# Kernel tuning notes

Hardware: AMD Instinct MI355X
Metric: run time of the kernel (lower is better)

The kernel has to match this reference:

```python
import jax, jax.numpy as jnp
import numpy as np

N, IN_F, OUT_F = 4096, 4096, 4096
THRESH = 0.05


def setup_inputs() -> dict:
    key = jax.random.key(0)
    k_x, k_w = jax.random.split(key)
    last_out = jax.random.normal(k_x, (N, IN_F), dtype=jnp.float32)
    # learned weight buffer, [out_features, in_features] like torch Linear
    weight = jax.random.normal(k_w, (OUT_F, IN_F), dtype=jnp.float32) * (1.0 / np.sqrt(IN_F))
    threshold = jnp.float32(THRESH)
    return {"last_out": last_out, "weight": weight, "threshold": threshold}


def reference(last_out, weight, threshold):
    # rtp_linear: runtime threshold pruning — activations with |x| <= threshold
    # are skipped (treated as zero) in the matmul. Bias buffer is unused
    # (dead code in the original forward).
    x = jnp.where(jnp.abs(last_out) > threshold, last_out, 0.0)
    # y[n, o] = sum_i x[n, i] * W[o, i]
    return jnp.einsum("ni,oi->no", x, weight)
```

## Files before the change

### kernel.cpp

```cpp
#include <hip/hip_runtime.h>
#include <hip/hip_bf16.h>

#define M_DIM 4096
#define N_DIM 4096
#define K_DIM 4096

typedef __attribute__((ext_vector_type(8))) __bf16 bf16x8;
typedef __attribute__((ext_vector_type(8))) short short8;
typedef __attribute__((ext_vector_type(8))) unsigned short ushort8;
typedef __attribute__((ext_vector_type(4))) float f32x4;

__device__ __forceinline__ void gload_lds16(const void* g, void* l) {
    __builtin_amdgcn_global_load_lds(
        (const __attribute__((address_space(1))) void*)g,
        (__attribute__((address_space(3))) void*)l,
        16, 0, 0);
}

__device__ __forceinline__ bf16x8 ld8(const unsigned short* p) {
    short8 r = *reinterpret_cast<const short8*>(p);
    return __builtin_bit_cast(bf16x8, r);
}

__global__ void prune_cvt2(const float* __restrict__ x,
                           const float* __restrict__ w,
                           unsigned short* __restrict__ xb,
                           unsigned short* __restrict__ wb,
                           const float* __restrict__ thrp, int n8) {
    const float thr = thrp[0];
    const int stride = gridDim.x * blockDim.x;
    const int total = 2 * n8;
    for (int idx = blockIdx.x * blockDim.x + threadIdx.x; idx < total; idx += stride) {
        const bool isx = idx < n8;
        const int j = isx ? idx : idx - n8;
        const float* src = isx ? x : w;
        unsigned short* dst = isx ? xb : wb;
        const float te = isx ? thr : -1.0f;
        const float4* p = reinterpret_cast<const float4*>(src) + 2 * (size_t)j;
        float4 v0 = p[0];
        float4 v1 = p[1];
        float v[8] = {v0.x, v0.y, v0.z, v0.w, v1.x, v1.y, v1.z, v1.w};
        ushort8 o;
#pragma unroll
        for (int e = 0; e < 8; ++e) {
            float f = v[e];
            f = (fabsf(f) > te) ? f : 0.0f;
            __hip_bfloat16 hh = __float2bfloat16(f);
            o[e] = *reinterpret_cast<unsigned short*>(&hh);
        }
        *reinterpret_cast<ushort8*>(dst + 8 * (size_t)j) = o;
    }
}

__global__ __launch_bounds__(512, 2) void gemm_8phase(
        const unsigned short* __restrict__ A,
        const unsigned short* __restrict__ B,
        float* __restrict__ C) {
    __shared__ __align__(16) unsigned short lds[65536];

    const int tid  = threadIdx.x;
    const int lane = tid & 63;
    const int wid  = tid >> 6;
    const int wr   = wid >> 2;
    const int wc   = wid & 3;

    const int bid = blockIdx.x;
    const int swz = (bid & 7) * 32 + (bid >> 3);
    const int bm = (swz >> 4) * 256;
    const int bn = (swz & 15) * 256;

    const int g  = tid & 255;
    const int ah = tid >> 8;
    const int arow = bm + ah * 128 + (g >> 3);
    const int acol = 8 * ((g & 7) ^ ((g >> 3) & 7));
    const unsigned short* Asrc = A + (size_t)arow * K_DIM + acol;
    const int AdstE = ah * 8192 + g * 8;

    const int h = lane + 64 * wr;
    const int brow = bn + wc * 64 + (h >> 3);
    const int bcol = 8 * ((h & 7) ^ ((h >> 3) & 7));
    const unsigned short* Bsrc = B + (size_t)brow * K_DIM + bcol;
    const int BdstE = wc * 4096 + h * 8;

#define SA(dstb, j, kg) gload_lds16(Asrc + (size_t)(32*(j))*K_DIM + (kg), (dstb) + AdstE + 2048*(j))
#define SB(dstb, j, kg) gload_lds16(Bsrc + (size_t)(16*(j))*K_DIM + (kg), (dstb) + BdstE + 1024*(j))

    const int fr  = lane & 15;
    const int kq4 = lane >> 4;
    const int rowOffA = (wr * 128 + fr) * 64;
    const int rowOffB = (wc * 64 + fr) * 64;
    const int sk0 = 8 * ((kq4    ) ^ (fr & 7));
    const int sk1 = 8 * ((kq4 + 4) ^ (fr & 7));

    f32x4 acc[8][4] = {};

    bf16x8 bfE[4][2], bfO[4][2];

#define MFMA16(q, BF, A00, A10, A01, A11)                                                          \
    __builtin_amdgcn_s_setprio(1);                                                                 \
    _Pragma("unroll")                                                                              \
    for (int n = 0; n < 4; ++n) {                                                                  \
        acc[2*(q)][n]   = __builtin_amdgcn_mfma_f32_16x16x32_bf16(A00, BF[n][0], acc[2*(q)][n], 0, 0, 0);   \
        acc[2*(q)+1][n] = __builtin_amdgcn_mfma_f32_16x16x32_bf16(A10, BF[n][0], acc[2*(q)+1][n], 0, 0, 0); \
    }                                                                                              \
    _Pragma("unroll")                                                                              \
    for (int n = 0; n < 4; ++n) {                                                                  \
        acc[2*(q)][n]   = __builtin_amdgcn_mfma_f32_16x16x32_bf16(A01, BF[n][1], acc[2*(q)][n], 0, 0, 0);   \
        acc[2*(q)+1][n] = __builtin_amdgcn_mfma_f32_16x16x32_bf16(A11, BF[n][1], acc[2*(q)+1][n], 0, 0, 0); \
    }                                                                                              \
    __builtin_amdgcn_s_setprio(0);

#define TILE_BODY(Ab, AbN, BbN, Bb, BFC, BFN, kna, knb)                                            \
    {                                                                                              \
                                                 \
        bf16x8 q00 = ld8((Ab) + rowOffA + 2 * 1024 + sk0);                                         \
        bf16x8 q10 = ld8((Ab) + rowOffA + 3 * 1024 + sk0);                                         \
        bf16x8 q01 = ld8((Ab) + rowOffA + 2 * 1024 + sk1);                                         \
        bf16x8 q11 = ld8((Ab) + rowOffA + 3 * 1024 + sk1);                                         \
        MFMA16(0, BFC, p00, p10, p01, p11);                                                        \
        asm volatile("s_waitcnt vmcnt(5)" ::: "memory");                                           \
        asm volatile("s_barrier" ::: "memory");                                                    \
                                            \
        bf16x8 r00 = ld8((Ab) + rowOffA + 4 * 1024 + sk0);                                         \
        bf16x8 r10 = ld8((Ab) + rowOffA + 5 * 1024 + sk0);                                         \
        bf16x8 r01 = ld8((Ab) + rowOffA + 4 * 1024 + sk1);                                         \
        bf16x8 r11 = ld8((Ab) + rowOffA + 5 * 1024 + sk1);                                         \
        SA((AbN), 0, (kna)); SA((AbN), 1, (kna));                                                  \
        MFMA16(1, BFC, q00, q10, q01, q11);                                                        \
        asm volatile("s_waitcnt vmcnt(6)" ::: "memory");                                           \
        asm volatile("s_barrier" ::: "memory");                                                    \
                                            \
        bf16x8 s00 = ld8((Ab) + rowOffA + 6 * 1024 + sk0);                                         \
        bf16x8 s10 = ld8((Ab) + rowOffA + 7 * 1024 + sk0);                                         \
        bf16x8 s01 = ld8((Ab) + rowOffA + 6 * 1024 + sk1);                                         \
        bf16x8 s11 = ld8((Ab) + rowOffA + 7 * 1024 + sk1);                                         \
        SA((AbN), 2, (kna)); SA((AbN), 3, (kna));                                                  \
        MFMA16(2, BFC, r00, r10, r01, r11);                                                        \
        asm volatile("s_waitcnt vmcnt(3)" ::: "memory");                                           \
        asm volatile("s_barrier" ::: "memory");                                                    \
                     \
        p00 = ld8((AbN) + rowOffA + 0 * 1024 + sk0);                                               \
        p10 = ld8((AbN) + rowOffA + 1 * 1024 + sk0);                                               \
        p01 = ld8((AbN) + rowOffA + 0 * 1024 + sk1);                                               \
        p11 = ld8((AbN) + rowOffA + 1 * 1024 + sk1);                                               \
        _Pragma("unroll")                                                                          \
        for (int n = 0; n < 4; ++n) {                                                              \
            BFN[n][0] = ld8((BbN) + rowOffB + n * 1024 + sk0);                                     \
            BFN[n][1] = ld8((BbN) + rowOffB + n * 1024 + sk1);                                     \
        }                                                                                          \
        SB((Bb), 0, (knb)); SB((Bb), 1, (knb)); SB((Bb), 2, (knb)); SB((Bb), 3, (knb));            \
        MFMA16(3, BFC, s00, s10, s01, s11);                                                        \
        asm volatile("s_waitcnt vmcnt(6)" ::: "memory");                                           \
        asm volatile("s_barrier" ::: "memory");                                                    \
    }

    unsigned short* A0 = lds;
    unsigned short* A1 = lds + 16384;
    unsigned short* B0 = lds + 32768;
    unsigned short* B1 = lds + 49152;

    SB(B0, 0, 0); SB(B0, 1, 0); SB(B0, 2, 0); SB(B0, 3, 0);
    SA(A0, 0, 0); SA(A0, 1, 0); SA(A0, 2, 0); SA(A0, 3, 0);
    SB(B1, 0, 64); SB(B1, 1, 64); SB(B1, 2, 64); SB(B1, 3, 64);
    asm volatile("s_waitcnt vmcnt(6)" ::: "memory");
    asm volatile("s_barrier" ::: "memory");

    bf16x8 p00 = ld8(A0 + rowOffA + 0 * 1024 + sk0);
    bf16x8 p10 = ld8(A0 + rowOffA + 1 * 1024 + sk0);
    bf16x8 p01 = ld8(A0 + rowOffA + 0 * 1024 + sk1);
    bf16x8 p11 = ld8(A0 + rowOffA + 1 * 1024 + sk1);
#pragma unroll
    for (int n = 0; n < 4; ++n) {
        bfE[n][0] = ld8(B0 + rowOffB + n * 1024 + sk0);
        bfE[n][1] = ld8(B0 + rowOffB + n * 1024 + sk1);
    }

    for (int t = 0; t < 64; t += 2) {
        const int kna0 = (t + 1) * 64;
        const int knb0 = (t + 2 < 64 ? t + 2 : 63) * 64;
        const int kna1 = (t + 2 < 64 ? t + 2 : 63) * 64;
        const int knb1 = (t + 3 < 64 ? t + 3 : 63) * 64;
        TILE_BODY(A0, A1, B1, B0, bfE, bfO, kna0, knb0);
        TILE_BODY(A1, A0, B0, B1, bfO, bfE, kna1, knb1);
    }

    asm volatile("s_waitcnt vmcnt(0)" ::: "memory");

    const int crow = bm + wr * 128 + kq4 * 4;
    const int ccol = bn + wc * 64 + fr;
#pragma unroll
    for (int m = 0; m < 8; ++m)
#pragma unroll
        for (int n = 0; n < 4; ++n)
#pragma unroll
            for (int j = 0; j < 4; ++j)
                C[(size_t)(crow + m * 16 + j) * N_DIM + ccol + n * 16] = acc[m][n][j];
}

__global__ void gemm_f32_fallback(const float* __restrict__ A,
                                  const float* __restrict__ B,
                                  float* __restrict__ C,
                                  const float* __restrict__ thrp) {
    __shared__ float As[32][33];
    __shared__ float Bs[32][33];
    const float thr = thrp[0];
    const int tx = threadIdx.x, ty = threadIdx.y;
    const int row = blockIdx.y * 32 + ty;
    float acc = 0.0f;
    for (int k0 = 0; k0 < K_DIM; k0 += 32) {
        float a = A[(size_t)row * K_DIM + k0 + tx];
        As[ty][tx] = (fabsf(a) > thr) ? a : 0.0f;
        Bs[ty][tx] = B[(size_t)(blockIdx.x * 32 + ty) * K_DIM + k0 + tx];
        __syncthreads();
#pragma unroll 8
        for (int kk = 0; kk < 32; ++kk)
            acc += As[ty][kk] * Bs[tx][kk];
        __syncthreads();
    }
    C[(size_t)row * N_DIM + blockIdx.x * 32 + tx] = acc;
}

extern "C" void kernel_launch(void* const* d_in, const int* in_sizes, int n_in,
                              void* d_out, int out_size, void* d_ws, size_t ws_size,
                              hipStream_t stream) {
    const float* x    = (const float*)d_in[0];
    const float* w    = (const float*)d_in[1];
    const float* thrp = (const float*)d_in[2];
    float* out = (float*)d_out;

    const size_t elems = (size_t)M_DIM * K_DIM;
    if (ws_size >= 2 * elems * sizeof(unsigned short)) {
        unsigned short* Ab = (unsigned short*)d_ws;
        unsigned short* Bb = Ab + elems;
        const int n8 = (int)(elems / 8);
        prune_cvt2<<<2048, 256, 0, stream>>>(x, w, Ab, Bb, thrp, n8);
        gemm_8phase<<<dim3(256), dim3(512), 0, stream>>>(Ab, Bb, out);
    } else {
        dim3 grid(N_DIM / 32, M_DIM / 32), blk(32, 32);
        gemm_f32_fallback<<<grid, blk, 0, stream>>>(x, w, out, thrp);
    }
}
```

Measured before the change: 156.1 us.

## Use 4 waves per block with 128x128 per-wave accumulator tiles

Changes the 256x256 GEMM block from 8 waves (each computing 128x64) to 4 waves (each computing 128x128), which doubles the accumulator registers and B fragments per wave. The goal is more MFMA work per LDS fragment load and fewer barriers per k-step, since the global-to-LDS staging pipeline and the wait counts are reorganized. The cost is heavy register pressure (256 accumulator VGPRs plus fragments), only 4 waves per CU at launch bounds (256,1), and less latency hiding.

```diff
diff --git a/kernel.cpp b/kernel.cpp
--- a/kernel.cpp
+++ b/kernel.cpp
@@ -52,7 +52,7 @@
     }
 }
 
-__global__ __launch_bounds__(512, 2) void gemm_8phase(
+__global__ __launch_bounds__(256, 1) void gemm_bigacc(
         const unsigned short* __restrict__ A,
         const unsigned short* __restrict__ B,
         float* __restrict__ C) {
@@ -61,96 +61,89 @@
     const int tid  = threadIdx.x;
     const int lane = tid & 63;
     const int wid  = tid >> 6;
-    const int wr   = wid >> 2;
-    const int wc   = wid & 3;
+    const int wr   = wid >> 1;
+    const int wc   = wid & 1;
 
     const int bid = blockIdx.x;
     const int swz = (bid & 7) * 32 + (bid >> 3);
     const int bm = (swz >> 4) * 256;
     const int bn = (swz & 15) * 256;
 
-    const int g  = tid & 255;
-    const int ah = tid >> 8;
-    const int arow = bm + ah * 128 + (g >> 3);
-    const int acol = 8 * ((g & 7) ^ ((g >> 3) & 7));
-    const unsigned short* Asrc = A + (size_t)arow * K_DIM + acol;
-    const int AdstE = ah * 8192 + g * 8;
-
-    const int h = lane + 64 * wr;
-    const int brow = bn + wc * 64 + (h >> 3);
-    const int bcol = 8 * ((h & 7) ^ ((h >> 3) & 7));
-    const unsigned short* Bsrc = B + (size_t)brow * K_DIM + bcol;
-    const int BdstE = wc * 4096 + h * 8;
-
-#define SA(dstb, j, kg) gload_lds16(Asrc + (size_t)(32*(j))*K_DIM + (kg), (dstb) + AdstE + 2048*(j))
-#define SB(dstb, j, kg) gload_lds16(Bsrc + (size_t)(16*(j))*K_DIM + (kg), (dstb) + BdstE + 1024*(j))
+    const int g = tid;
+    const int srow = g >> 3;
+    const int scol = 8 * ((g & 7) ^ (srow & 7));
+    const unsigned short* Asrc = A + (size_t)(bm + srow) * K_DIM + scol;
+    const unsigned short* Bsrc = B + (size_t)(bn + srow) * K_DIM + scol;
+    const int dstE = g * 8;
+
+#define SA(dstb, j, kg) gload_lds16(Asrc + (size_t)(32*(j))*K_DIM + (kg), (dstb) + 2048*(j) + dstE)
+#define SB(dstb, j, kg) gload_lds16(Bsrc + (size_t)(32*(j))*K_DIM + (kg), (dstb) + 2048*(j) + dstE)
 
     const int fr  = lane & 15;
     const int kq4 = lane >> 4;
     const int rowOffA = (wr * 128 + fr) * 64;
-    const int rowOffB = (wc * 64 + fr) * 64;
+    const int rowOffB = (wc * 128 + fr) * 64;
     const int sk0 = 8 * ((kq4    ) ^ (fr & 7));
     const int sk1 = 8 * ((kq4 + 4) ^ (fr & 7));
 
-    f32x4 acc[8][4] = {};
-
-    bf16x8 bfE[4][2], bfO[4][2];
-
-#define MFMA16(q, BF, A00, A10, A01, A11)                                                          \
+    f32x4 acc[8][8] = {};
+
+    bf16x8 bfE[8][2], bfO[8][2];
+
+#define MFMA32(q, BF, A00, A10, A01, A11)                                                          \
     __builtin_amdgcn_s_setprio(1);                                                                 \
     _Pragma("unroll")                                                                              \
-    for (int n = 0; n < 4; ++n) {                                                                  \
+    for (int n = 0; n < 8; ++n) {                                                                  \
         acc[2*(q)][n]   = __builtin_amdgcn_mfma_f32_16x16x32_bf16(A00, BF[n][0], acc[2*(q)][n], 0, 0, 0);   \
         acc[2*(q)+1][n] = __builtin_amdgcn_mfma_f32_16x16x32_bf16(A10, BF[n][0], acc[2*(q)+1][n], 0, 0, 0); \
     }                                                                                              \
     _Pragma("unroll")                                                                              \
-    for (int n = 0; n < 4; ++n) {                                                                  \
+    for (int n = 0; n < 8; ++n) {                                                                  \
         acc[2*(q)][n]   = __builtin_amdgcn_mfma_f32_16x16x32_bf16(A01, BF[n][1], acc[2*(q)][n], 0, 0, 0);   \
         acc[2*(q)+1][n] = __builtin_amdgcn_mfma_f32_16x16x32_bf16(A11, BF[n][1], acc[2*(q)+1][n], 0, 0, 0); \
     }                                                                                              \
     __builtin_amdgcn_s_setprio(0);
 
-#define TILE_BODY(Ab, AbN, BbN, Bb, BFC, BFN, kna, knb)                                            \
+#define TILE_BODY(Ab, Bb, AbN, BbN, BFC, BFN, kn)                                                  \
     {                                                                                              \
-                                                 \
+                            \
         bf16x8 q00 = ld8((Ab) + rowOffA + 2 * 1024 + sk0);                                         \
         bf16x8 q10 = ld8((Ab) + rowOffA + 3 * 1024 + sk0);                                         \
         bf16x8 q01 = ld8((Ab) + rowOffA + 2 * 1024 + sk1);                                         \
         bf16x8 q11 = ld8((Ab) + rowOffA + 3 * 1024 + sk1);                                         \
-        MFMA16(0, BFC, p00, p10, p01, p11);                                                        \
-        asm volatile("s_waitcnt vmcnt(5)" ::: "memory");                                           \
-        asm volatile("s_barrier" ::: "memory");                                                    \
+        SB((BbN), 0, (kn)); SB((BbN), 1, (kn)); SB((BbN), 2, (kn)); SB((BbN), 3, (kn));            \
+        SB((BbN), 4, (kn)); SB((BbN), 5, (kn)); SB((BbN), 6, (kn)); SB((BbN), 7, (kn));            \
+        SA((AbN), 0, (kn)); SA((AbN), 4, (kn));                                                    \
+        MFMA32(0, BFC, p00, p10, p01, p11);                                                        \
                                             \
         bf16x8 r00 = ld8((Ab) + rowOffA + 4 * 1024 + sk0);                                         \
         bf16x8 r10 = ld8((Ab) + rowOffA + 5 * 1024 + sk0);                                         \
         bf16x8 r01 = ld8((Ab) + rowOffA + 4 * 1024 + sk1);                                         \
         bf16x8 r11 = ld8((Ab) + rowOffA + 5 * 1024 + sk1);                                         \
-        SA((AbN), 0, (kna)); SA((AbN), 1, (kna));                                                  \
-        MFMA16(1, BFC, q00, q10, q01, q11);                                                        \
-        asm volatile("s_waitcnt vmcnt(6)" ::: "memory");                                           \
+        SA((AbN), 1, (kn)); SA((AbN), 5, (kn));                                                    \
+        MFMA32(1, BFC, q00, q10, q01, q11);                                                        \
+        asm volatile("s_waitcnt vmcnt(2)" ::: "memory");                                           \
         asm volatile("s_barrier" ::: "memory");                                                    \
                                             \
         bf16x8 s00 = ld8((Ab) + rowOffA + 6 * 1024 + sk0);                                         \
         bf16x8 s10 = ld8((Ab) + rowOffA + 7 * 1024 + sk0);                                         \
         bf16x8 s01 = ld8((Ab) + rowOffA + 6 * 1024 + sk1);                                         \
         bf16x8 s11 = ld8((Ab) + rowOffA + 7 * 1024 + sk1);                                         \
-        SA((AbN), 2, (kna)); SA((AbN), 3, (kna));                                                  \
-        MFMA16(2, BFC, r00, r10, r01, r11);                                                        \
-        asm volatile("s_waitcnt vmcnt(3)" ::: "memory");                                           \
-        asm volatile("s_barrier" ::: "memory");                                                    \
-                     \
+        SA((AbN), 2, (kn)); SA((AbN), 6, (kn));                                                    \
+        MFMA32(2, BFC, r00, r10, r01, r11);                                                        \
+                   \
         p00 = ld8((AbN) + rowOffA + 0 * 1024 + sk0);                                               \
         p10 = ld8((AbN) + rowOffA + 1 * 1024 + sk0);                                               \
         p01 = ld8((AbN) + rowOffA + 0 * 1024 + sk1);                                               \
         p11 = ld8((AbN) + rowOffA + 1 * 1024 + sk1);                                               \
         _Pragma("unroll")                                                                          \
-        for (int n = 0; n < 4; ++n) {                                                              \
+        for (int n = 0; n < 8; ++n) {                                                              \
             BFN[n][0] = ld8((BbN) + rowOffB + n * 1024 + sk0);                                     \
             BFN[n][1] = ld8((BbN) + rowOffB + n * 1024 + sk1);                                     \
         }                                                                                          \
-        SB((Bb), 0, (knb)); SB((Bb), 1, (knb)); SB((Bb), 2, (knb)); SB((Bb), 3, (knb));            \
-        MFMA16(3, BFC, s00, s10, s01, s11);                                                        \
-        asm volatile("s_waitcnt vmcnt(6)" ::: "memory");                                           \
+        SA((AbN), 3, (kn)); SA((AbN), 7, (kn));                                                    \
+        MFMA32(3, BFC, s00, s10, s01, s11);                                                        \
+        asm volatile("s_waitcnt vmcnt(2)" ::: "memory");                                           \
         asm volatile("s_barrier" ::: "memory");                                                    \
     }
 
@@ -160,9 +153,10 @@
     unsigned short* B1 = lds + 49152;
 
     SB(B0, 0, 0); SB(B0, 1, 0); SB(B0, 2, 0); SB(B0, 3, 0);
-    SA(A0, 0, 0); SA(A0, 1, 0); SA(A0, 2, 0); SA(A0, 3, 0);
-    SB(B1, 0, 64); SB(B1, 1, 64); SB(B1, 2, 64); SB(B1, 3, 64);
-    asm volatile("s_waitcnt vmcnt(6)" ::: "memory");
+    SB(B0, 4, 0); SB(B0, 5, 0); SB(B0, 6, 0); SB(B0, 7, 0);
+    SA(A0, 0, 0); SA(A0, 4, 0); SA(A0, 1, 0); SA(A0, 5, 0);
+    SA(A0, 2, 0); SA(A0, 6, 0); SA(A0, 3, 0); SA(A0, 7, 0);
+    asm volatile("s_waitcnt vmcnt(2)" ::: "memory");
     asm volatile("s_barrier" ::: "memory");
 
     bf16x8 p00 = ld8(A0 + rowOffA + 0 * 1024 + sk0);
@@ -170,28 +164,26 @@
     bf16x8 p01 = ld8(A0 + rowOffA + 0 * 1024 + sk1);
     bf16x8 p11 = ld8(A0 + rowOffA + 1 * 1024 + sk1);
 #pragma unroll
-    for (int n = 0; n < 4; ++n) {
+    for (int n = 0; n < 8; ++n) {
         bfE[n][0] = ld8(B0 + rowOffB + n * 1024 + sk0);
         bfE[n][1] = ld8(B0 + rowOffB + n * 1024 + sk1);
     }
 
     for (int t = 0; t < 64; t += 2) {
-        const int kna0 = (t + 1) * 64;
-        const int knb0 = (t + 2 < 64 ? t + 2 : 63) * 64;
-        const int kna1 = (t + 2 < 64 ? t + 2 : 63) * 64;
-        const int knb1 = (t + 3 < 64 ? t + 3 : 63) * 64;
-        TILE_BODY(A0, A1, B1, B0, bfE, bfO, kna0, knb0);
-        TILE_BODY(A1, A0, B0, B1, bfO, bfE, kna1, knb1);
+        const int kn0 = (t + 1) * 64;
+        const int kn1 = (t + 2 < 64 ? t + 2 : 63) * 64;
+        TILE_BODY(A0, B0, A1, B1, bfE, bfO, kn0);
+        TILE_BODY(A1, B1, A0, B0, bfO, bfE, kn1);
     }
 
     asm volatile("s_waitcnt vmcnt(0)" ::: "memory");
 
     const int crow = bm + wr * 128 + kq4 * 4;
-    const int ccol = bn + wc * 64 + fr;
+    const int ccol = bn + wc * 128 + fr;
 #pragma unroll
     for (int m = 0; m < 8; ++m)
 #pragma unroll
-        for (int n = 0; n < 4; ++n)
+        for (int n = 0; n < 8; ++n)
 #pragma unroll
             for (int j = 0; j < 4; ++j)
                 C[(size_t)(crow + m * 16 + j) * N_DIM + ccol + n * 16] = acc[m][n][j];
@@ -234,7 +226,7 @@
         unsigned short* Bb = Ab + elems;
         const int n8 = (int)(elems / 8);
         prune_cvt2<<<2048, 256, 0, stream>>>(x, w, Ab, Bb, thrp, n8);
-        gemm_8phase<<<dim3(256), dim3(512), 0, stream>>>(Ab, Bb, out);
+        gemm_bigacc<<<dim3(256), dim3(256), 0, stream>>>(Ab, Bb, out);
     } else {
         dim3 grid(N_DIM / 32, M_DIM / 32), blk(32, 32);
         gemm_f32_fallback<<<grid, blk, 0, stream>>>(x, w, out, thrp);
```

After: 284.7 us. 82.4% more time.
